# Kernel optimization log

Hardware: AMD Instinct MI355X
Metric: run time of the kernel (lower is better)

Reference implementation:

```python
import jax, jax.numpy as jnp
import numpy as np

N = 20000      # atoms
E = 320000     # edges
F = 128        # node_size (hard-pinned by split(128) / expand to 384)
RBF = 20
RC = 5.0
ITERS = 3
NM = 64        # molecules in batch


def setup_inputs() -> dict:
    key = jax.random.key(0)
    ks = iter(jax.random.split(key, 64))
    def nrm(shape, scale=0.05):
        return jax.random.normal(next(ks), shape, dtype=jnp.float32) * scale
    inp = {}
    inp["z"] = jax.random.randint(next(ks), (N,), 0, 119)
    inp["graph"] = jax.random.randint(next(ks), (E, 2), 0, N)
    inp["edges_dist"] = jax.random.uniform(next(ks), (E,), minval=0.5, maxval=RC, dtype=jnp.float32)
    sense = jax.random.normal(next(ks), (E, 3), dtype=jnp.float32)
    inp["edges_sense"] = sense / jnp.linalg.norm(sense, axis=1, keepdims=True)
    inp["graph_idx"] = jnp.sort(jax.random.randint(next(ks), (N,), 0, NM))
    # parameters (stacked over ITERS message/update blocks)
    inp["emb"] = nrm((119, F), 1.0)
    inp["mw1"] = nrm((ITERS, F, F)); inp["mb1"] = nrm((ITERS, F))
    inp["mw2"] = nrm((ITERS, 3 * F, F)); inp["mb2"] = nrm((ITERS, 3 * F))
    inp["ew"] = nrm((ITERS, 3 * F, RBF)); inp["eb"] = nrm((ITERS, 3 * F))
    inp["uw"] = nrm((ITERS, F, F)); inp["vw"] = nrm((ITERS, F, F))
    inp["aw1"] = nrm((ITERS, F, 2 * F)); inp["ab1"] = nrm((ITERS, F))
    inp["aw2"] = nrm((ITERS, 3 * F, F)); inp["ab2"] = nrm((ITERS, 3 * F))
    inp["ow1"] = nrm((F, F)); inp["ob1"] = nrm((F,))
    inp["ow2"] = nrm((1, F)); inp["ob2"] = nrm((1,))
    return inp


def reference(z, graph, edges_dist, edges_sense, graph_idx,
              emb, mw1, mb1, mw2, mb2, ew, eb,
              uw, vw, aw1, ab1, aw2, ab2, ow1, ob1, ow2, ob2):
    src = graph[:, 0]   # scatter target (index_add index)
    dst = graph[:, 1]   # gather source (neighbour)
    s = emb[z]                                  # [N, F]
    v = jnp.zeros((N, 3, F), dtype=s.dtype)     # [N, 3, F]
    # edge-level precompute (same every iteration)
    n = jnp.arange(1, RBF + 1, dtype=jnp.float32)
    d = edges_dist[:, None]
    rbf = jnp.sin(n * jnp.pi * d / RC) / d                              # [E, RBF]
    cut = 0.5 * (jnp.cos(jnp.pi * edges_dist / RC) + 1.0) * (edges_dist < RC)  # [E]
    for i in range(ITERS):
        # --- Message block ---
        a = jax.nn.silu(s @ mw1[i].T + mb1[i]) @ mw2[i].T + mb2[i]      # [N, 3F]
        dist_rep = (rbf @ ew[i].T + eb[i]) * cut[:, None]               # [E, 3F]
        res = a[dst] * dist_rep                                         # [E, 3F]
        rv, rs, rd = res[:, :F], res[:, F:2 * F], res[:, 2 * F:]
        resv = v[dst] * rv[:, None, :] + edges_sense[:, :, None] * rd[:, None, :]  # [E,3,F]
        s = s + 2.0 * jax.ops.segment_sum(rs, src, num_segments=N)
        v = v + 2.0 * jax.ops.segment_sum(resv, src, num_segments=N)
        # --- Update block ---
        Uv = v @ uw[i].T                                                # [N,3,F]
        Vv = v @ vw[i].T
        h = jnp.concatenate([s, jnp.linalg.norm(Vv, axis=1)], axis=-1)  # [N, 2F]
        a2 = jax.nn.silu(h @ aw1[i].T + ab1[i]) @ aw2[i].T + ab2[i]     # [N, 3F]
        avv, asv, ass = a2[:, :F], a2[:, F:2 * F], a2[:, 2 * F:]
        s = s + ass + asv * jnp.sum(Uv * Vv, axis=1)
        v = v + avv[:, None, :] * Uv
    out = jax.nn.silu(s @ ow1.T + ob1) @ ow2.T + ob2                    # [N, 1]
    return jax.ops.segment_sum(out, graph_idx, num_segments=NM)         # [NM, 1]
```

## Files before the change

kernel.cpp:

```cpp
#include <hip/hip_runtime.h>
#include <math.h>

#define NN 20000
#define NE 320000
#define FD 128
#define RBFN 20
#define RC_ 5.0f
#define NITER 3
#define NMOL 64
#define F3 384
#define F2 256
#define PI_ 3.14159265358979323846f
#define KB 128
#define LPAD 8
#define SDS 392
#define BM2 32

typedef __attribute__((ext_vector_type(8))) short  bf16x8;
typedef __attribute__((ext_vector_type(4))) float  floatx4;
typedef unsigned short u16;
typedef unsigned int   u32;

__device__ __forceinline__ u16 f2b(float x) {
    union { float f; unsigned int u; } v; v.f = x;
    unsigned int u = v.u;
    return (u16)((u + 0x7fffu + ((u >> 16) & 1u)) >> 16);
}
__device__ __forceinline__ float b2f(u16 x) {
    union { unsigned int u; float f; } v; v.u = ((unsigned int)x) << 16;
    return v.f;
}
__device__ __forceinline__ float blo(u32 w) {
    union { unsigned int u; float f; } v; v.u = w << 16; return v.f;
}
__device__ __forceinline__ float bhi(u32 w) {
    union { unsigned int u; float f; } v; v.u = w & 0xffff0000u; return v.f;
}
__device__ __forceinline__ u32 pack2(float a, float b) {
    return (u32)f2b(a) | ((u32)f2b(b) << 16);
}

__global__ __launch_bounds__(256) void init_all_kernel(
    const float* s0, int n0, const float* s1, int n1, const float* s2, int n2,
    const float* s3, int n3, const float* s4, int n4, const float* s5, int n5,
    const float* s6, int n6, u16* __restrict__ wdst,
    const float* __restrict__ ew, u16* __restrict__ ewb,
    const int* __restrict__ z, const float* __restrict__ emb,
    float* __restrict__ s, u16* __restrict__ sbf,
    float* __restrict__ v_a, int* __restrict__ v_pk_i, int* __restrict__ cnt,
    float* __restrict__ out)
{
    int idx = blockIdx.x * 256 + threadIdx.x;
    if (idx < NN * F3) v_a[idx] = 0.f;
    if (idx < NN * F3 / 2) v_pk_i[idx] = 0;
    if (idx < NN) cnt[idx] = 0;
    if (idx < NMOL) out[idx] = 0.f;
    if (idx < NN * FD) {
        int n = idx >> 7, f = idx & 127;
        float v = emb[z[n] * FD + f];
        s[idx] = v; sbf[idx] = f2b(v);
    }
    if (idx < NITER * F3 * 32) {
        int k = idx & 31;
        int row = idx >> 5;
        ewb[idx] = (k < RBFN) ? f2b(ew[row * RBFN + k]) : (u16)0;
    }
    {
        int w = idx;
        u16* dst = wdst;
        if (w < n0) { dst[w] = f2b(s0[w]); return; } w -= n0; dst += n0;
        if (w < n1) { dst[w] = f2b(s1[w]); return; } w -= n1; dst += n1;
        if (w < n2) { dst[w] = f2b(s2[w]); return; } w -= n2; dst += n2;
        if (w < n3) { dst[w] = f2b(s3[w]); return; } w -= n3; dst += n3;
        if (w < n4) { dst[w] = f2b(s4[w]); return; } w -= n4; dst += n4;
        if (w < n5) { dst[w] = f2b(s5[w]); return; } w -= n5; dst += n5;
        if (w < n6) { dst[w] = f2b(s6[w]); }
    }
}

__global__ __launch_bounds__(256) void csr_count_kernel(const int* __restrict__ graph,
    int* __restrict__ cnt)
{
    int e = blockIdx.x * 256 + threadIdx.x;
    if (e >= NE) return;
    atomicAdd(&cnt[graph[2 * e]], 1);
}

__global__ __launch_bounds__(1024) void csr_scan_kernel(const int* __restrict__ cnt,
    int* __restrict__ row_ptr, int* __restrict__ cursor)
{
    __shared__ int sd[1024];
    int tid = threadIdx.x;
    const int chunk = (NN + 1023) / 1024;
    int start = tid * chunk;
    int end = start + chunk; if (end > NN) end = NN;
    int sum = 0;
    for (int j = start; j < end; j++) sum += cnt[j];
    sd[tid] = sum;
    __syncthreads();
    for (int off = 1; off < 1024; off <<= 1) {
        int v = 0;
        if (tid >= off) v = sd[tid - off];
        __syncthreads();
        if (tid >= off) sd[tid] += v;
        __syncthreads();
    }
    int run = (tid == 0) ? 0 : sd[tid - 1];
    for (int j = start; j < end; j++) {
        row_ptr[j] = run;
        cursor[j]  = run;
        run += cnt[j];
    }
    if (tid == 0) row_ptr[NN] = NE;
}

__global__ __launch_bounds__(256) void csr_scatter_kernel(const int* __restrict__ graph,
    int* __restrict__ cursor, int* __restrict__ edge_list)
{
    int e = blockIdx.x * 256 + threadIdx.x;
    if (e >= NE) return;
    int p = atomicAdd(&cursor[graph[2 * e]], 1);
    edge_list[p] = e;
}

__global__ __launch_bounds__(256) void edge_stream_kernel(
    const int* __restrict__ edge_list, const int* __restrict__ graph,
    const float* __restrict__ dist, const float* __restrict__ sense,
    u16* __restrict__ rbf_bf, float* __restrict__ cut_p,
    float* __restrict__ sense_p, int* __restrict__ dst_p)
{
    int j = blockIdx.x * 256 + threadIdx.x;
    if (j >= NE) return;
    int e = edge_list[j];
    float d = dist[e];
    float inv = 1.f / d;
    float base = PI_ * d / RC_;
    float s1, c1;
    __sincosf(base, &s1, &c1);
    float twoc = c1 + c1;
    u16 tmp[32];
    float sprev = 0.f, scur = s1;
    #pragma unroll
    for (int k = 0; k < RBFN; k++) {
        tmp[k] = f2b(scur * inv);
        float snext = twoc * scur - sprev;
        sprev = scur; scur = snext;
    }
    #pragma unroll
    for (int k = RBFN; k < 32; k++) tmp[k] = 0;
    u16* rb = rbf_bf + (size_t)j * 32;
    #pragma unroll
    for (int x = 0; x < 32; x += 8)
        *(bf16x8*)&rb[x] = *(const bf16x8*)&tmp[x];
    cut_p[j] = 0.5f * (c1 + 1.f) * (d < RC_ ? 1.f : 0.f);
    dst_p[j] = graph[2 * e + 1];
    sense_p[3 * j + 0] = sense[3 * e + 0];
    sense_p[3 * j + 1] = sense[3 * e + 1];
    sense_p[3 * j + 2] = sense[3 * e + 2];
}

__global__ __launch_bounds__(256) void mlp1_kernel(const u16* __restrict__ A,
    const u16* __restrict__ W1, const float* __restrict__ b1,
    const u16* __restrict__ W2, const float* __restrict__ b2,
    u16* __restrict__ Ob, int M)
{
    __shared__ u16 As[BM2][KB + LPAD];
    __shared__ u16 Ws[128][KB + LPAD];
    u16 (*T)[KB + LPAD] = &Ws[64];
    const int bm = blockIdx.x * BM2;
    const int tid = threadIdx.x;
    const int wave = tid >> 6, lane = tid & 63;
    const int wrow = (wave >> 1) * 16;
    const int wn1  = (wave & 1) * 64;
    const int wn   = (wave & 1) * 32;
    const int quad = lane >> 4, lr = lane & 15;
    const int r = tid >> 2, q = tid & 3;
    const int r3 = tid >> 3, c16 = (tid & 7) * 16;

    floatx4 acc1[4];
    #pragma unroll
    for (int j = 0; j < 4; j++) acc1[j] = (floatx4)0.f;

    {
        int gm = bm + r3;
        u16* dA = &As[r3][c16];
        if (gm < M) {
            const u16* ap = A + (size_t)gm * KB + c16;
            *(bf16x8*)&dA[0] = *(const bf16x8*)(ap);
            *(bf16x8*)&dA[8] = *(const bf16x8*)(ap + 8);
        } else {
            *(bf16x8*)&dA[0] = (bf16x8)0;
            *(bf16x8*)&dA[8] = (bf16x8)0;
        }
        #pragma unroll
        for (int h = 0; h < 2; h++) {
            int wr = r + h * 64;
            const u16* wp = W1 + (size_t)wr * KB + q * 32;
            u16* dW = &Ws[wr][q * 32];
            #pragma unroll
            for (int x = 0; x < 32; x += 8)
                *(bf16x8*)&dW[x] = *(const bf16x8*)(wp + x);
        }
    }
    __syncthreads();
    #pragma unroll
    for (int kk = 0; kk < KB; kk += 32) {
        bf16x8 a0 = *(const bf16x8*)&As[wrow + lr][kk + quad * 8];
        #pragma unroll
        for (int j = 0; j < 4; j++) {
            bf16x8 b = *(const bf16x8*)&Ws[wn1 + j * 16 + lr][kk + quad * 8];
            acc1[j] = __builtin_amdgcn_mfma_f32_16x16x32_bf16(a0, b, acc1[j], 0, 0, 0);
        }
    }
    __syncthreads();
    #pragma unroll
    for (int j = 0; j < 4; j++) {
        int col = wn1 + j * 16 + lr;
        float bb = b1[col];
        #pragma unroll
        for (int rr = 0; rr < 4; rr++) {
            int row = wrow + quad * 4 + rr;
            float v = acc1[j][rr] + bb;
            v = v / (1.f + __expf(-v));
            T[row][col] = f2b(v);
        }
    }
    for (int pp = 0; pp < 6; pp++) {
        const int c0 = pp * 64;
        {
            const u16* wp = W2 + (size_t)(c0 + r) * KB + q * 32;
            u16* dW = &Ws[r][q * 32];
            #pragma unroll
            for (int x = 0; x < 32; x += 8)
                *(bf16x8*)&dW[x] = *(const bf16x8*)(wp + x);
        }
        __syncthreads();
        floatx4 acc2[2];
        #pragma unroll
        for (int j = 0; j < 2; j++) acc2[j] = (floatx4)0.f;
        #pragma unroll
        for (int kk = 0; kk < KB; kk += 32) {
            bf16x8 a0 = *(const bf16x8*)&T[wrow + lr][kk + quad * 8];
            bf16x8 b0 = *(const bf16x8*)&Ws[wn + lr     ][kk + quad * 8];
            bf16x8 b1 = *(const bf16x8*)&Ws[wn + 16 + lr][kk + quad * 8];
            acc2[0] = __builtin_amdgcn_mfma_f32_16x16x32_bf16(a0, b0, acc2[0], 0, 0, 0);
            acc2[1] = __builtin_amdgcn_mfma_f32_16x16x32_bf16(a0, b1, acc2[1], 0, 0, 0);
        }
        #pragma unroll
        for (int j = 0; j < 2; j++) {
            int gn = c0 + wn + j * 16 + lr;
            float bb = b2[gn];
            #pragma unroll
            for (int rr = 0; rr < 4; rr++) {
                int gm = bm + wrow + quad * 4 + rr;
                if (gm < M) {
                    u16 val = f2b(acc2[j][rr] + bb);
                    int off = (gn < 256) ? ((gn & 127) * 2 + (gn >> 7))
                                         : (256 + (gn & 127));
                    Ob[(size_t)gm * F3 + off] = val;
                }
            }
        }
        __syncthreads();
    }
}

__global__ __launch_bounds__(256) void gemm_uv(const u16* __restrict__ A,
    const u16* __restrict__ Wu, const u16* __restrict__ Wv,
    u16* __restrict__ U, u16* __restrict__ V, int M)
{
    __shared__ u16 As[BM2][KB + LPAD];
    __shared__ u16 Bu[64][KB + LPAD];
    __shared__ u16 Bv[64][KB + LPAD];
    const int bm = blockIdx.x * BM2;
    const int tid = threadIdx.x;
    const int r = tid >> 2;
    const int q = tid & 3;
    const int r3 = tid >> 3, c16 = (tid & 7) * 16;
    const int wave = tid >> 6;
    const int lane = tid & 63;
    const int wrow = (wave >> 1) * 16;
    const int wn = (wave & 1) * 32;
    const int quad = lane >> 4;
    const int lr = lane & 15;

    {
        int gm = bm + r3;
        u16* dA = &As[r3][c16];
        if (gm < M) {
            const u16* ap = A + (size_t)gm * KB + c16;
            *(bf16x8*)&dA[0] = *(const bf16x8*)(ap);
            *(bf16x8*)&dA[8] = *(const bf16x8*)(ap + 8);
        } else {
            *(bf16x8*)&dA[0] = (bf16x8)0;
            *(bf16x8*)&dA[8] = (bf16x8)0;
        }
    }

    #pragma unroll
    for (int bn = 0; bn < FD; bn += 64) {
        {
            int gn = bn + r;
            const u16* up = Wu + (size_t)gn * KB + q * 32;
            const u16* vp = Wv + (size_t)gn * KB + q * 32;
            u16* dU = &Bu[r][q * 32];
            u16* dV = &Bv[r][q * 32];
            #pragma unroll
            for (int x = 0; x < 32; x += 8) {
                *(bf16x8*)&dU[x] = *(const bf16x8*)(up + x);
                *(bf16x8*)&dV[x] = *(const bf16x8*)(vp + x);
            }
        }
        __syncthreads();
        floatx4 au[2], av[2];
        #pragma unroll
        for (int j = 0; j < 2; j++) { au[j] = (floatx4)0.f; av[j] = (floatx4)0.f; }
        #pragma unroll
        for (int kk = 0; kk < KB; kk += 32) {
            bf16x8 a0 = *(const bf16x8*)&As[wrow + lr][kk + quad * 8];
            bf16x8 u0 = *(const bf16x8*)&Bu[wn + lr     ][kk + quad * 8];
            bf16x8 u1 = *(const bf16x8*)&Bu[wn + 16 + lr][kk + quad * 8];
            bf16x8 v0 = *(const bf16x8*)&Bv[wn + lr     ][kk + quad * 8];
            bf16x8 v1 = *(const bf16x8*)&Bv[wn + 16 + lr][kk + quad * 8];
            au[0] = __builtin_amdgcn_mfma_f32_16x16x32_bf16(a0, u0, au[0], 0, 0, 0);
            au[1] = __builtin_amdgcn_mfma_f32_16x16x32_bf16(a0, u1, au[1], 0, 0, 0);
            av[0] = __builtin_amdgcn_mfma_f32_16x16x32_bf16(a0, v0, av[0], 0, 0, 0);
            av[1] = __builtin_amdgcn_mfma_f32_16x16x32_bf16(a0, v1, av[1], 0, 0, 0);
        }
        #pragma unroll
        for (int j = 0; j < 2; j++) {
            int gn = bn + wn + j * 16 + lr;
            #pragma unroll
            for (int rr = 0; rr < 4; rr++) {
                int gm = bm + wrow + quad * 4 + rr;
                if (gm < M) {
                    U[(size_t)gm * FD + gn] = f2b(au[j][rr]);
                    V[(size_t)gm * FD + gn] = f2b(av[j][rr]);
                }
            }
        }
        __syncthreads();
    }
}

__global__ __launch_bounds__(256) void edge_mfma_kernel(
    const u16* __restrict__ rbf_bf, const float* __restrict__ cut_p,
    const float* __restrict__ sense_p, const int* __restrict__ dst_p,
    const u16* __restrict__ ewb, const float* __restrict__ eb,
    const u16* __restrict__ a_pk, const float* __restrict__ s_in,
    const float* __restrict__ v_in, const u16* __restrict__ v_pk,
    const int* __restrict__ row_ptr,
    float* __restrict__ s_out, u16* __restrict__ s_obf,
    float* __restrict__ v_out, u16* __restrict__ v_obf)
{
    __shared__ u16   sdrep[16 * SDS];
    __shared__ float scut[16];
    __shared__ float ssen[16][4];
    __shared__ int   sdst[16];
    __shared__ float red[4 * 128];

    const int n = blockIdx.x;
    const int tid = threadIdx.x;
    const int wave = tid >> 6;
    const int lane = tid & 63;
    const int quad = lane >> 4;
    const int lr = lane & 15;
    const int f = tid & 127;
    const int half = tid >> 7;

    int beg = row_ptr[n], end = row_ptr[n + 1];
    float accs = 0.f, accv0 = 0.f, accv1 = 0.f, accv2 = 0.f;

    for (int t0 = beg; t0 < end; t0 += 16) {
        int cnt = end - t0; if (cnt > 16) cnt = 16;
        __syncthreads();
        if (tid < 16) {
            scut[tid] = (tid < cnt) ? cut_p[t0 + tid] : 0.f;
            sdst[tid] = (tid < cnt) ? dst_p[t0 + tid] : 0;
        }
        if (tid >= 64 && tid < 64 + 3 * cnt) {
            int x = tid - 64;
            ssen[x / 3][x % 3] = sense_p[3 * t0 + x];
        }
        bf16x8 afrag;
        int ge = t0 + lr;
        if (ge < end) afrag = *(const bf16x8*)&rbf_bf[(size_t)ge * 32 + quad * 8];
        else          afrag = (bf16x8)0;
        floatx4 dacc[6];
        #pragma unroll
        for (int nt = 0; nt < 6; nt++) {
            int nrow = (wave * 6 + nt) * 16 + lr;
            bf16x8 bfrag = *(const bf16x8*)&ewb[(size_t)nrow * 32 + quad * 8];
            dacc[nt] = __builtin_amdgcn_mfma_f32_16x16x32_bf16(afrag, bfrag, (floatx4)0.f, 0, 0, 0);
        }
        __syncthreads();
        #pragma unroll
        for (int nt = 0; nt < 6; nt++) {
            int ncol = (wave * 6 + nt) * 16 + lr;
            float ebn = eb[ncol];
            #pragma unroll
            for (int rr = 0; rr < 4; rr++) {
                int e = quad * 4 + rr;
                sdrep[e * SDS + ncol] = f2b((dacc[nt][rr] + ebn) * scut[e]);
            }
        }
        __syncthreads();
        int nh = cnt - half * 8; if (nh > 8) nh = 8;
        for (int k = 0; k < nh; k++) {
            int e = half * 8 + k;
            int dst = sdst[e];
            const u16* sr = &sdrep[e * SDS];
            float drv = b2f(sr[f]);
            float drs = b2f(sr[FD + f]);
            float drd = b2f(sr[2 * FD + f]);
            const u16* ar = a_pk + (size_t)dst * F3;
            u32 ap = *(const u32*)(ar + f * 2);
            float rv = b2f((u16)(ap & 0xffff)) * drv;
            float rs = b2f((u16)(ap >> 16))    * drs;
            float rd = b2f(ar[256 + f])        * drd;
            accs += rs;
            const u16* vr = v_pk + (size_t)dst * F3;
            u32 vp = *(const u32*)(vr + f * 2);
            accv0 += b2f((u16)(vp & 0xffff)) * rv + ssen[e][0] * rd;
            accv1 += b2f((u16)(vp >> 16))    * rv + ssen[e][1] * rd;
            accv2 += b2f(vr[256 + f])        * rv + ssen[e][2] * rd;
        }
    }
    __syncthreads();
    if (half == 1) {
        red[f] = accs; red[128 + f] = accv0; red[256 + f] = accv1; red[384 + f] = accv2;
    }
    __syncthreads();
    if (half == 0) {
        accs  += red[f];       accv0 += red[128 + f];
        accv1 += red[256 + f]; accv2 += red[384 + f];
        int nb = n * FD + f;
        float so = s_in[nb] + 2.f * accs;
        s_out[nb] = so; s_obf[nb] = f2b(so);
        int vb = n * F3 + f;
        float w0 = v_in[vb]           + 2.f * accv0;
        float w1 = v_in[vb + FD]      + 2.f * accv1;
        float w2 = v_in[vb + 2 * FD]  + 2.f * accv2;
        v_out[vb]          = w0; v_obf[vb]          = f2b(w0);
        v_out[vb + FD]     = w1; v_obf[vb + FD]     = f2b(w1);
        v_out[vb + 2 * FD] = w2; v_obf[vb + 2 * FD] = f2b(w2);
    }
}

template<bool LAST>
__global__ __launch_bounds__(256) void mlp2_update_next_kernel(
    const u16* __restrict__ sbf_mid, const float* __restrict__ s_mid,
    const float* __restrict__ v_mid,
    const u16* __restrict__ Uv, const u16* __restrict__ Vv,
    const u16* __restrict__ W1, const float* __restrict__ b1,
    const u16* __restrict__ W2, const float* __restrict__ b2,
    float* __restrict__ s_out,
    float* __restrict__ v_out, u16* __restrict__ v_pk,
    const u16* __restrict__ N_W1, const float* __restrict__ N_b1,
    const u16* __restrict__ N_W2, const float* __restrict__ N_b2,
    u16* __restrict__ a_pk,
    const u16* __restrict__ H_W1, const float* __restrict__ H_b1,
    const float* __restrict__ ow2, const float* __restrict__ ob2,
    const int* __restrict__ gidx, float* __restrict__ outp, int M)
{
    __shared__ u16 As[BM2][KB + LPAD];
    __shared__ u16 Ws[128][KB + LPAD];
    u16 (*T)[KB + LPAD] = &Ws[64];
    const int bm = blockIdx.x * BM2;
    const int tid = threadIdx.x;
    const int wave = tid >> 6, lane = tid & 63;
    const int wrow = (wave >> 1) * 16;
    const int wn1  = (wave & 1) * 64;
    const int wn   = (wave & 1) * 32;
    const int quad = lane >> 4, lr = lane & 15;
    const int r = tid >> 2, q = tid & 3;
    const int r3 = tid >> 3, c16 = (tid & 7) * 16;

    floatx4 acc1[4];
    #pragma unroll
    for (int j = 0; j < 4; j++) acc1[j] = (floatx4)0.f;

    {
        int gm = bm + r3;
        u16* dA = &As[r3][c16];
        if (gm < M) {
            const u16* ap = sbf_mid + (size_t)gm * FD + c16;
            *(bf16x8*)&dA[0] = *(const bf16x8*)(ap);
            *(bf16x8*)&dA[8] = *(const bf16x8*)(ap + 8);
        } else {
            *(bf16x8*)&dA[0] = (bf16x8)0;
            *(bf16x8*)&dA[8] = (bf16x8)0;
        }
        #pragma unroll
        for (int h = 0; h < 2; h++) {
            int wr = r + h * 64;
            const u16* wp = W1 + (size_t)wr * F2 + q * 32;
            u16* dW = &Ws[wr][q * 32];
            #pragma unroll
            for (int x = 0; x < 32; x += 8)
                *(bf16x8*)&dW[x] = *(const bf16x8*)(wp + x);
        }
    }
    __syncthreads();
    #pragma unroll
    for (int kk = 0; kk < KB; kk += 32) {
        bf16x8 a0 = *(const bf16x8*)&As[wrow + lr][kk + quad * 8];
        #pragma unroll
        for (int j = 0; j < 4; j++) {
            bf16x8 b = *(const bf16x8*)&Ws[wn1 + j * 16 + lr][kk + quad * 8];
            acc1[j] = __builtin_amdgcn_mfma_f32_16x16x32_bf16(a0, b, acc1[j], 0, 0, 0);
        }
    }
    __syncthreads();
    {
        int gm = bm + r3;
        u16* dA = &As[r3][c16];
        if (gm < M) {
            const u16* vvp = Vv + (size_t)gm * F3 + c16;
            #pragma unroll
            for (int t = 0; t < 2; t++) {
                bf16x8 c0 = *(const bf16x8*)(vvp + t * 8);
                bf16x8 c1 = *(const bf16x8*)(vvp + FD + t * 8);
                bf16x8 c2 = *(const bf16x8*)(vvp + 2 * FD + t * 8);
                #pragma unroll
                for (int x = 0; x < 8; x++) {
                    float a = b2f((u16)c0[x]);
                    float b = b2f((u16)c1[x]);
                    float c = b2f((u16)c2[x]);
                    dA[t * 8 + x] = f2b(sqrtf(a * a + b * b + c * c));
                }
            }
        } else {
            *(bf16x8*)&dA[0] = (bf16x8)0;
            *(bf16x8*)&dA[8] = (bf16x8)0;
        }
        #pragma unroll
        for (int h = 0; h < 2; h++) {
            int wr = r + h * 64;
            const u16* wp = W1 + (size_t)wr * F2 + KB + q * 32;
            u16* dW = &Ws[wr][q * 32];
            #pragma unroll
            for (int x = 0; x < 32; x += 8)
                *(bf16x8*)&dW[x] = *(const bf16x8*)(wp + x);
        }
    }
    __syncthreads();
    #pragma unroll
    for (int kk = 0; kk < KB; kk += 32) {
        bf16x8 a0 = *(const bf16x8*)&As[wrow + lr][kk + quad * 8];
        #pragma unroll
        for (int j = 0; j < 4; j++) {
            bf16x8 b = *(const bf16x8*)&Ws[wn1 + j * 16 + lr][kk + quad * 8];
            acc1[j] = __builtin_amdgcn_mfma_f32_16x16x32_bf16(a0, b, acc1[j], 0, 0, 0);
        }
    }
    __syncthreads();
    #pragma unroll
    for (int j = 0; j < 4; j++) {
        int col = wn1 + j * 16 + lr;
        float bb = b1[col];
        #pragma unroll
        for (int rr = 0; rr < 4; rr++) {
            int row = wrow + quad * 4 + rr;
            float v = acc1[j][rr] + bb;
            v = v / (1.f + __expf(-v));
            T[row][col] = f2b(v);
        }
    }

    float avvr[2][4], asvr[2][4];
    #pragma unroll
    for (int pp = 0; pp < 6; pp++) {
        const int part  = pp / 3;
        const int piece = pp % 3;
        const int c0 = piece * 128 + part * 64;
        {
            const u16* wp = W2 + (size_t)(c0 + r) * KB + q * 32;
            u16* dW = &Ws[r][q * 32];
            #pragma unroll
            for (int x = 0; x < 32; x += 8)
                *(bf16x8*)&dW[x] = *(const bf16x8*)(wp + x);
        }
        __syncthreads();
        floatx4 acc2[2];
        #pragma unroll
        for (int j = 0; j < 2; j++) acc2[j] = (floatx4)0.f;
        #pragma unroll
        for (int kk = 0; kk < KB; kk += 32) {
            bf16x8 a0 = *(const bf16x8*)&T[wrow + lr][kk + quad * 8];
            bf16x8 b0 = *(const bf16x8*)&Ws[wn + lr     ][kk + quad * 8];
            bf16x8 b1 = *(const bf16x8*)&Ws[wn + 16 + lr][kk + quad * 8];
            acc2[0] = __builtin_amdgcn_mfma_f32_16x16x32_bf16(a0, b0, acc2[0], 0, 0, 0);
            acc2[1] = __builtin_amdgcn_mfma_f32_16x16x32_bf16(a0, b1, acc2[1], 0, 0, 0);
        }
        if (piece == 0) {
            #pragma unroll
            for (int j = 0; j < 2; j++) {
                int gn = c0 + wn + j * 16 + lr;
                float bb = b2[gn];
                #pragma unroll
                for (int rr = 0; rr < 4; rr++)
                    avvr[j][rr] = acc2[j][rr] + bb;
            }
        } else if (piece == 1) {
            #pragma unroll
            for (int j = 0; j < 2; j++) {
                int gn = c0 + wn + j * 16 + lr;
                float bb = b2[gn];
                #pragma unroll
                for (int rr = 0; rr < 4; rr++)
                    asvr[j][rr] = acc2[j][rr] + bb;
            }
        } else {
            #pragma unroll
            for (int j = 0; j < 2; j++) {
                int gn = c0 + wn + j * 16 + lr;
                int f  = gn - 256;
                float bb = b2[gn];
                #pragma unroll
                for (int rr = 0; rr < 4; rr++) {
                    int row = wrow + quad * 4 + rr;
                    int gm = bm + row;
                    if (gm < M) {
                        float ass = acc2[j][rr] + bb;
                        float asv = asvr[j][rr];
                        float avv = avvr[j][rr];
                        int vb = gm * F3 + f;
                        float u0 = b2f(Uv[vb]);
                        float u1 = b2f(Uv[vb + FD]);
                        float u2 = b2f(Uv[vb + 2 * FD]);
                        float w0 = b2f(Vv[vb]);
                        float w1 = b2f(Vv[vb + FD]);
                        float w2 = b2f(Vv[vb + 2 * FD]);
                        float dot = u0 * w0 + u1 * w1 + u2 * w2;
                        int nb = gm * FD + f;
                        float so = s_mid[nb] + ass + asv * dot;
                        s_out[nb] = so;
                        As[row][f] = f2b(so);
                        float y0 = v_mid[vb]          + avv * u0;
                        float y1 = v_mid[vb + FD]     + avv * u1;
                        float y2 = v_mid[vb + 2 * FD] + avv * u2;
                        v_out[vb]          = y0;
                        v_out[vb + FD]     = y1;
                        v_out[vb + 2 * FD] = y2;
                        char* vpb = (char*)v_pk + (size_t)gm * (2 * F3);
                        *(u32*)(vpb + 4 * f) = pack2(y0, y1);
                        *(u16*)(vpb + 512 + 2 * f) = f2b(y2);
                    } else {
                        As[row][f] = 0;
                    }
                }
            }
        }
        __syncthreads();
    }

    if constexpr (!LAST) {
        {
            #pragma unroll
            for (int h = 0; h < 2; h++) {
                int wr = r + h * 64;
                const u16* wp = N_W1 + (size_t)wr * KB + q * 32;
                u16* dW = &Ws[wr][q * 32];
                #pragma unroll
                for (int x = 0; x < 32; x += 8)
                    *(bf16x8*)&dW[x] = *(const bf16x8*)(wp + x);
            }
        }
        __syncthreads();
        #pragma unroll
        for (int j = 0; j < 4; j++) acc1[j] = (floatx4)0.f;
        #pragma unroll
        for (int kk = 0; kk < KB; kk += 32) {
            bf16x8 a0 = *(const bf16x8*)&As[wrow + lr][kk + quad * 8];
            #pragma unroll
            for (int j = 0; j < 4; j++) {
                bf16x8 b = *(const bf16x8*)&Ws[wn1 + j * 16 + lr][kk + quad * 8];
                acc1[j] = __builtin_amdgcn_mfma_f32_16x16x32_bf16(a0, b, acc1[j], 0, 0, 0);
            }
        }
        __syncthreads();
        #pragma unroll
        for (int j = 0; j < 4; j++) {
            int col = wn1 + j * 16 + lr;
            float bb = N_b1[col];
            #pragma unroll
            for (int rr = 0; rr < 4; rr++) {
                int row = wrow + quad * 4 + rr;
                float v = acc1[j][rr] + bb;
                v = v / (1.f + __expf(-v));
                T[row][col] = f2b(v);
            }
        }
        for (int pp = 0; pp < 6; pp++) {
            const int c0 = pp * 64;
            {
                const u16* wp = N_W2 + (size_t)(c0 + r) * KB + q * 32;
                u16* dW = &Ws[r][q * 32];
                #pragma unroll
                for (int x = 0; x < 32; x += 8)
                    *(bf16x8*)&dW[x] = *(const bf16x8*)(wp + x);
            }
            __syncthreads();
            floatx4 acc2[2];
            #pragma unroll
            for (int j = 0; j < 2; j++) acc2[j] = (floatx4)0.f;
            #pragma unroll
            for (int kk = 0; kk < KB; kk += 32) {
                bf16x8 a0 = *(const bf16x8*)&T[wrow + lr][kk + quad * 8];
                bf16x8 b0 = *(const bf16x8*)&Ws[wn + lr     ][kk + quad * 8];
                bf16x8 b1 = *(const bf16x8*)&Ws[wn + 16 + lr][kk + quad * 8];
                acc2[0] = __builtin_amdgcn_mfma_f32_16x16x32_bf16(a0, b0, acc2[0], 0, 0, 0);
                acc2[1] = __builtin_amdgcn_mfma_f32_16x16x32_bf16(a0, b1, acc2[1], 0, 0, 0);
            }
            #pragma unroll
            for (int j = 0; j < 2; j++) {
                int gn = c0 + wn + j * 16 + lr;
                float bb = N_b2[gn];
                #pragma unroll
                for (int rr = 0; rr < 4; rr++) {
                    int gm = bm + wrow + quad * 4 + rr;
                    if (gm < M) {
                        u16 val = f2b(acc2[j][rr] + bb);
                        int off = (gn < 256) ? ((gn & 127) * 2 + (gn >> 7))
                                             : (256 + (gn & 127));
                        a_pk[(size_t)gm * F3 + off] = val;
                    }
                }
            }
            __syncthreads();
        }
    } else {
        {
            #pragma unroll
            for (int h = 0; h < 2; h++) {
                int wr = r + h * 64;
                const u16* wp = H_W1 + (size_t)wr * KB + q * 32;
                u16* dW = &Ws[wr][q * 32];
                #pragma unroll
                for (int x = 0; x < 32; x += 8)
                    *(bf16x8*)&dW[x] = *(const bf16x8*)(wp + x);
            }
        }
        __syncthreads();
        #pragma unroll
        for (int j = 0; j < 4; j++) acc1[j] = (floatx4)0.f;
        #pragma unroll
        for (int kk = 0; kk < KB; kk += 32) {
            bf16x8 a0 = *(const bf16x8*)&As[wrow + lr][kk + quad * 8];
            #pragma unroll
            for (int j = 0; j < 4; j++) {
                bf16x8 b = *(const bf16x8*)&Ws[wn1 + j * 16 + lr][kk + quad * 8];
                acc1[j] = __builtin_amdgcn_mfma_f32_16x16x32_bf16(a0, b, acc1[j], 0, 0, 0);
            }
        }
        __syncthreads();
        float* ow2s = (float*)&As[0][0];
        if (tid < KB) ow2s[tid] = ow2[tid];
        #pragma unroll
        for (int j = 0; j < 4; j++) {
            int col = wn1 + j * 16 + lr;
            float bb = H_b1[col];
            #pragma unroll
            for (int rr = 0; rr < 4; rr++) {
                int row = wrow + quad * 4 + rr;
                float v = acc1[j][rr] + bb;
                v = v / (1.f + __expf(-v));
                T[row][col] = f2b(v);
            }
        }
        __syncthreads();
        int nl = tid >> 3, seg = tid & 7;
        float v = 0.f;
        #pragma unroll
        for (int x = 0; x < 16; x++) {
            int col = seg * 16 + x;
            v += b2f(T[nl][col]) * ow2s[col];
        }
        v += __shfl_down(v, 4);
        v += __shfl_down(v, 2);
        v += __shfl_down(v, 1);
        if (seg == 0) {
            int gm = bm + nl;
            if (gm < M) atomicAdd(&outp[gidx[gm]], v + ob2[0]);
        }
    }
}

extern "C" void kernel_launch(void* const* d_in, const int* in_sizes, int n_in,
                              void* d_out, int out_size, void* d_ws, size_t ws_size,
                              hipStream_t stream)
{
    const int*   z     = (const int*)d_in[0];
    const int*   graph = (const int*)d_in[1];
    const float* dist  = (const float*)d_in[2];
    const float* sense = (const float*)d_in[3];
    const int*   gidx  = (const int*)d_in[4];
    const float* emb   = (const float*)d_in[5];
    const float* mw1   = (const float*)d_in[6];
    const float* mb1   = (const float*)d_in[7];
    const float* mw2   = (const float*)d_in[8];
    const float* mb2   = (const float*)d_in[9];
    const float* ew    = (const float*)d_in[10];
    const float* eb    = (const float*)d_in[11];
    const float* uw    = (const float*)d_in[12];
    const float* vw    = (const float*)d_in[13];
    const float* aw1   = (const float*)d_in[14];
    const float* ab1   = (const float*)d_in[15];
    const float* aw2   = (const float*)d_in[16];
    const float* ab2   = (const float*)d_in[17];
    const float* ow1   = (const float*)d_in[18];
    const float* ob1   = (const float*)d_in[19];
    const float* ow2   = (const float*)d_in[20];
    const float* ob2   = (const float*)d_in[21];
    float* out = (float*)d_out;

    float* W = (float*)d_ws;
    float* s_a    = W; W += (size_t)NN * FD;
    float* s_b    = W; W += (size_t)NN * FD;
    float* v_a    = W; W += (size_t)NN * F3;
    float* v_b    = W; W += (size_t)NN * F3;
    float* cut_p  = W; W += (size_t)NE;
    float* sns_p  = W; W += (size_t)NE * 3;
    float* nodeval= W; W += (size_t)NN;
    u16* U = (u16*)W;
    u16* sbf_a = U; U += (size_t)NN * FD;
    u16* sbf_b = U; U += (size_t)NN * FD;
    u16* vbf_b = U; U += (size_t)NN * F3;
    u16* a_pk  = U; U += (size_t)NN * F3;
    u16* v_pk  = U; U += (size_t)NN * F3;
    u16* h_bf  = U; U += (size_t)NN * F2;
    u16* a2_bf = U; U += (size_t)NN * F3;
    u16* Uv_bf = U; U += (size_t)NN * F3;
    u16* Vv_bf = U; U += (size_t)NN * F3;
    u16* rbf_bf= U; U += (size_t)NE * 32;
    u16* ewb   = U; U += (size_t)NITER * F3 * 32;
    u16* wb    = U; U += 557056;
    int* ip = (int*)U;
    int* row_ptr   = ip; ip += NN + 1;
    int* cnt       = ip; ip += NN;
    int* cursor    = ip; ip += NN;
    int* edge_list = ip; ip += NE;
    int* dst_p     = ip; ip += NE;

    u16* wb_mw1 = wb;
    u16* wb_mw2 = wb + 49152;
    u16* wb_uw  = wb + 196608;
    u16* wb_vw  = wb + 245760;
    u16* wb_aw1 = wb + 294912;
    u16* wb_aw2 = wb + 393216;
    u16* wb_ow1 = wb + 540672;

    const int TB = 256;
    dim3 b256(TB);

    init_all_kernel<<<dim3((NN * F3 + TB - 1) / TB), b256, 0, stream>>>(
        mw1, 49152, mw2, 147456, uw, 49152, vw, 49152, aw1, 98304, aw2, 147456,
        ow1, 16384, wb, ew, ewb, z, emb, s_a, sbf_a, v_a, (int*)v_pk, cnt, out);
    csr_count_kernel<<<dim3((NE + TB - 1) / TB), b256, 0, stream>>>(graph, cnt);
    csr_scan_kernel<<<dim3(1), dim3(1024), 0, stream>>>(cnt, row_ptr, cursor);
    csr_scatter_kernel<<<dim3((NE + TB - 1) / TB), b256, 0, stream>>>(graph, cursor, edge_list);
    edge_stream_kernel<<<dim3((NE + TB - 1) / TB), b256, 0, stream>>>(
        edge_list, graph, dist, sense, rbf_bf, cut_p, sns_p, dst_p);

    dim3 gM2((NN + BM2 - 1) / BM2);
    dim3 gUV((3 * NN + BM2 - 1) / BM2);

    mlp1_kernel<<<gM2, b256, 0, stream>>>(sbf_a,
        wb_mw1, mb1, wb_mw2, mb2, a_pk, NN);

    for (int i = 0; i < NITER; i++) {
        edge_mfma_kernel<<<dim3(NN), b256, 0, stream>>>(
            rbf_bf, cut_p, sns_p, dst_p,
            ewb + (size_t)i * F3 * 32, eb + (size_t)i * F3,
            a_pk, s_a, v_a, v_pk, row_ptr, s_b, sbf_b, v_b, vbf_b);
        gemm_uv<<<gUV, b256, 0, stream>>>(vbf_b, wb_uw + (size_t)i * FD * FD,
            wb_vw + (size_t)i * FD * FD, Uv_bf, Vv_bf, 3 * NN);
        if (i < NITER - 1) {
            mlp2_update_next_kernel<false><<<gM2, b256, 0, stream>>>(
                sbf_b, s_b, v_b, Uv_bf, Vv_bf,
                wb_aw1 + (size_t)i * FD * F2, ab1 + (size_t)i * FD,
                wb_aw2 + (size_t)i * F3 * FD, ab2 + (size_t)i * F3,
                s_a, v_a, v_pk,
                wb_mw1 + (size_t)(i + 1) * FD * FD, mb1 + (size_t)(i + 1) * FD,
                wb_mw2 + (size_t)(i + 1) * F3 * FD, mb2 + (size_t)(i + 1) * F3, a_pk,
                nullptr, nullptr, nullptr, nullptr, nullptr, nullptr, NN);
        } else {
            mlp2_update_next_kernel<true><<<gM2, b256, 0, stream>>>(
                sbf_b, s_b, v_b, Uv_bf, Vv_bf,
                wb_aw1 + (size_t)i * FD * F2, ab1 + (size_t)i * FD,
                wb_aw2 + (size_t)i * F3 * FD, ab2 + (size_t)i * F3,
                s_a, v_a, v_pk,
                nullptr, nullptr, nullptr, nullptr, nullptr,
                wb_ow1, ob1, ow2, ob2, gidx, out, NN);
        }
    }
}
```

Baseline: 934.5 us.

## Split edge kernel over feature halves and hierarchically reduce molecule outputs

```diff
diff --git a/kernel.cpp b/kernel.cpp
--- a/kernel.cpp
+++ b/kernel.cpp
@@ -13,7 +13,7 @@
 #define PI_ 3.14159265358979323846f
 #define KB 128
 #define LPAD 8
-#define SDS 392
+#define SDS2 200
 #define BM2 32
 
 typedef __attribute__((ext_vector_type(8))) short  bf16x8;
@@ -343,7 +343,7 @@
     }
 }
 
-__global__ __launch_bounds__(256) void edge_mfma_kernel(
+__global__ __launch_bounds__(128) void edge_mfma_kernel(
     const u16* __restrict__ rbf_bf, const float* __restrict__ cut_p,
     const float* __restrict__ sense_p, const int* __restrict__ dst_p,
     const u16* __restrict__ ewb, const float* __restrict__ eb,
@@ -353,20 +353,22 @@
     float* __restrict__ s_out, u16* __restrict__ s_obf,
     float* __restrict__ v_out, u16* __restrict__ v_obf)
 {
-    __shared__ u16   sdrep[16 * SDS];
+    __shared__ u16   sdrep[16 * SDS2];
     __shared__ float scut[16];
     __shared__ float ssen[16][4];
     __shared__ int   sdst[16];
-    __shared__ float red[4 * 128];
+    __shared__ float red[4 * 64];
 
     const int n = blockIdx.x;
+    const int h = blockIdx.y;
     const int tid = threadIdx.x;
     const int wave = tid >> 6;
     const int lane = tid & 63;
     const int quad = lane >> 4;
     const int lr = lane & 15;
-    const int f = tid & 127;
-    const int half = tid >> 7;
+    const int fl = tid & 63;
+    const int fg = h * 64 + fl;
+    const int grp = tid >> 6;
 
     int beg = row_ptr[n], end = row_ptr[n + 1];
     float accs = 0.f, accv0 = 0.f, accv1 = 0.f, accv2 = 0.f;
@@ -389,55 +391,60 @@
         floatx4 dacc[6];
         #pragma unroll
         for (int nt = 0; nt < 6; nt++) {
-            int nrow = (wave * 6 + nt) * 16 + lr;
+            int tt = wave * 6 + nt;
+            int comp = tt >> 2, sub = tt & 3;
+            int nrow = comp * 128 + h * 64 + sub * 16 + lr;
             bf16x8 bfrag = *(const bf16x8*)&ewb[(size_t)nrow * 32 + quad * 8];
             dacc[nt] = __builtin_amdgcn_mfma_f32_16x16x32_bf16(afrag, bfrag, (floatx4)0.f, 0, 0, 0);
         }
         __syncthreads();
         #pragma unroll
         for (int nt = 0; nt < 6; nt++) {
-            int ncol = (wave * 6 + nt) * 16 + lr;
-            float ebn = eb[ncol];
+            int tt = wave * 6 + nt;
+            int comp = tt >> 2, sub = tt & 3;
+            int ncg = comp * 128 + h * 64 + sub * 16 + lr;
+            int lc  = comp * 64 + sub * 16 + lr;
+            float ebn = eb[ncg];
             #pragma unroll
             for (int rr = 0; rr < 4; rr++) {
                 int e = quad * 4 + rr;
-                sdrep[e * SDS + ncol] = f2b((dacc[nt][rr] + ebn) * scut[e]);
-            }
-        }
-        __syncthreads();
-        int nh = cnt - half * 8; if (nh > 8) nh = 8;
+                sdrep[e * SDS2 + lc] = f2b((dacc[nt][rr] + ebn) * scut[e]);
+            }
+        }
+        __syncthreads();
+        int nh = cnt - grp * 8; if (nh > 8) nh = 8;
         for (int k = 0; k < nh; k++) {
-            int e = half * 8 + k;
+            int e = grp * 8 + k;
             int dst = sdst[e];
-            const u16* sr = &sdrep[e * SDS];
-            float drv = b2f(sr[f]);
-            float drs = b2f(sr[FD + f]);
-            float drd = b2f(sr[2 * FD + f]);
+            const u16* sr = &sdrep[e * SDS2];
+            float drv = b2f(sr[fl]);
+            float drs = b2f(sr[64 + fl]);
+            float drd = b2f(sr[128 + fl]);
             const u16* ar = a_pk + (size_t)dst * F3;
-            u32 ap = *(const u32*)(ar + f * 2);
+            u32 ap = *(const u32*)(ar + fg * 2);
             float rv = b2f((u16)(ap & 0xffff)) * drv;
             float rs = b2f((u16)(ap >> 16))    * drs;
-            float rd = b2f(ar[256 + f])        * drd;
+            float rd = b2f(ar[256 + fg])       * drd;
             accs += rs;
             const u16* vr = v_pk + (size_t)dst * F3;
-            u32 vp = *(const u32*)(vr + f * 2);
+            u32 vp = *(const u32*)(vr + fg * 2);
             accv0 += b2f((u16)(vp & 0xffff)) * rv + ssen[e][0] * rd;
             accv1 += b2f((u16)(vp >> 16))    * rv + ssen[e][1] * rd;
-            accv2 += b2f(vr[256 + f])        * rv + ssen[e][2] * rd;
-        }
-    }
-    __syncthreads();
-    if (half == 1) {
-        red[f] = accs; red[128 + f] = accv0; red[256 + f] = accv1; red[384 + f] = accv2;
-    }
-    __syncthreads();
-    if (half == 0) {
-        accs  += red[f];       accv0 += red[128 + f];
-        accv1 += red[256 + f]; accv2 += red[384 + f];
-        int nb = n * FD + f;
+            accv2 += b2f(vr[256 + fg])       * rv + ssen[e][2] * rd;
+        }
+    }
+    __syncthreads();
+    if (grp == 1) {
+        red[fl] = accs; red[64 + fl] = accv0; red[128 + fl] = accv1; red[192 + fl] = accv2;
+    }
+    __syncthreads();
+    if (grp == 0) {
+        accs  += red[fl];       accv0 += red[64 + fl];
+        accv1 += red[128 + fl]; accv2 += red[192 + fl];
+        int nb = n * FD + fg;
         float so = s_in[nb] + 2.f * accs;
         s_out[nb] = so; s_obf[nb] = f2b(so);
-        int vb = n * F3 + f;
+        int vb = n * F3 + fg;
         float w0 = v_in[vb]           + 2.f * accv0;
         float w1 = v_in[vb + FD]      + 2.f * accv1;
         float w2 = v_in[vb + 2 * FD]  + 2.f * accv2;
@@ -461,7 +468,7 @@
     u16* __restrict__ a_pk,
     const u16* __restrict__ H_W1, const float* __restrict__ H_b1,
     const float* __restrict__ ow2, const float* __restrict__ ob2,
-    const int* __restrict__ gidx, float* __restrict__ outp, int M)
+    float* __restrict__ nodeval, int M)
 {
     __shared__ u16 As[BM2][KB + LPAD];
     __shared__ u16 Ws[128][KB + LPAD];
@@ -782,9 +789,22 @@
         v += __shfl_down(v, 1);
         if (seg == 0) {
             int gm = bm + nl;
-            if (gm < M) atomicAdd(&outp[gidx[gm]], v + ob2[0]);
-        }
-    }
+            if (gm < M) nodeval[gm] = v + ob2[0];
+        }
+    }
+}
+
+__global__ __launch_bounds__(256) void mol_reduce_kernel(const float* __restrict__ nodeval,
+    const int* __restrict__ gidx, float* __restrict__ out)
+{
+    __shared__ float mol[NMOL];
+    int tid = threadIdx.x;
+    if (tid < NMOL) mol[tid] = 0.f;
+    __syncthreads();
+    int x = blockIdx.x * 256 + tid;
+    if (x < NN) atomicAdd(&mol[gidx[x]], nodeval[x]);
+    __syncthreads();
+    if (tid < NMOL && mol[tid] != 0.f) atomicAdd(&out[tid], mol[tid]);
 }
 
 extern "C" void kernel_launch(void* const* d_in, const int* in_sizes, int n_in,
@@ -865,12 +885,13 @@
 
     dim3 gM2((NN + BM2 - 1) / BM2);
     dim3 gUV((3 * NN + BM2 - 1) / BM2);
+    dim3 gE(NN, 2);
 
     mlp1_kernel<<<gM2, b256, 0, stream>>>(sbf_a,
         wb_mw1, mb1, wb_mw2, mb2, a_pk, NN);
 
     for (int i = 0; i < NITER; i++) {
-        edge_mfma_kernel<<<dim3(NN), b256, 0, stream>>>(
+        edge_mfma_kernel<<<gE, dim3(128), 0, stream>>>(
             rbf_bf, cut_p, sns_p, dst_p,
             ewb + (size_t)i * F3 * 32, eb + (size_t)i * F3,
             a_pk, s_a, v_a, v_pk, row_ptr, s_b, sbf_b, v_b, vbf_b);
@@ -884,7 +905,7 @@
                 s_a, v_a, v_pk,
                 wb_mw1 + (size_t)(i + 1) * FD * FD, mb1 + (size_t)(i + 1) * FD,
                 wb_mw2 + (size_t)(i + 1) * F3 * FD, mb2 + (size_t)(i + 1) * F3, a_pk,
-                nullptr, nullptr, nullptr, nullptr, nullptr, nullptr, NN);
+                nullptr, nullptr, nullptr, nullptr, nullptr, NN);
         } else {
             mlp2_update_next_kernel<true><<<gM2, b256, 0, stream>>>(
                 sbf_b, s_b, v_b, Uv_bf, Vv_bf,
@@ -892,7 +913,9 @@
                 wb_aw2 + (size_t)i * F3 * FD, ab2 + (size_t)i * F3,
                 s_a, v_a, v_pk,
                 nullptr, nullptr, nullptr, nullptr, nullptr,
-                wb_ow1, ob1, ow2, ob2, gidx, out, NN);
-        }
-    }
-}
+                wb_ow1, ob1, ow2, ob2, nodeval, NN);
+        }
+    }
+
+    mol_reduce_kernel<<<dim3((NN + TB - 1) / TB), b256, 0, stream>>>(nodeval, gidx, out);
+}
```

Measured after the change: 811.4 us, median of 2. 1.15x faster.
